# Optimization experiments

Measured on AMD Instinct MI355X. Metric: run time of the kernel, lower is better.

## Reference

```python
import jax, jax.numpy as jnp
import numpy as np

D, K, CIN, CD, COUT = 3, 16, 128, 32, 256
C = CIN + CD                  # 160 = C_in + C_delta after concat
DM = -(-COUT // C)            # depth_multiplier = ceil(C_out / C) = 2
N, I = 4, 2048                # batch, points per cloud; M = N*I = 8192


def _bn(x, g, b, eps=1e-5):
    # BatchNorm1d in training mode: biased batch statistics over dim 0
    mu = x.mean(0)
    v = x.var(0)
    return (x - mu) * jax.lax.rsqrt(v + eps) * g + b


def _knn(p, k):
    # knn_graph over ALL M points (wrapper passes no batch vector), loop=True
    d2 = jnp.sum(p * p, axis=1)
    dist = d2[:, None] + d2[None, :] - 2.0 * (p @ p.T)   # [M,M]
    _, idx = jax.lax.top_k(-dist, k)                     # [M,K], self first
    return idx


def _gconv(t, w, b, M):
    # grouped Conv1d(K, K*K, kernel=K, groups=K): t [M,K,K], w [K(cin), K(out/grp), K(tap)]
    return jnp.einsum('mcl,col->mco', t, w).reshape(M, K * K) + b


def _xconv(xf, pf, idx, w1a, b1a, g1a, be1a, w1b, b1b, g1b, be1b,
           w2, b2, g2a, be2a, wc2a, bc2a, g2b, be2b, wc2b, bc2b, g2c, be2c,
           wcd, bcd, wl, bl):
    M = pf.shape[0]
    rel = pf[idx] - pf[:, None, :]                       # [M,K,D] relative neighbor coords
    # mlp1: lift relative coords to C_delta features
    h = rel.reshape(M * K, D)
    h = _bn(jax.nn.elu(h @ w1a + b1a), g1a, be1a)
    h = _bn(jax.nn.elu(h @ w1b + b1b), g1b, be1b)
    x_star = jnp.concatenate([h.reshape(M, K, CD), xf[idx]], axis=-1)  # [M,K,C]
    x_star = x_star.transpose(0, 2, 1)                   # [M,C,K]
    # mlp2: learn KxK X-transformation from the K*D relative coords
    t = _bn(jax.nn.elu(rel.reshape(M, K * D) @ w2 + b2), g2a, be2a).reshape(M, K, K)
    t = _bn(jax.nn.elu(_gconv(t, wc2a, bc2a, M)), g2b, be2b).reshape(M, K, K)
    t = _bn(_gconv(t, wc2b, bc2b, M), g2c, be2c).reshape(M, K, K)
    xt = jnp.einsum('mck,mkj->mcj', x_star, t)           # [M,C,K] batched matmul
    # depthwise Conv1d(C, C*DM, K, groups=C) collapses K, then final Linear
    y = jnp.einsum('mcl,col->mco', xt, wcd).reshape(M, C * DM) + bcd
    return y @ wl + bl                                   # [M,COUT]


def setup_inputs() -> dict:
    key = jax.random.key(0)
    ks = jax.random.split(key, 16)
    r = lambda k, s: jax.random.normal(k, s, jnp.float32) * 0.1
    return dict(
        x=jax.random.normal(ks[0], (N, I, CIN), jnp.float32),
        pos=jax.random.normal(ks[1], (N, I, D), jnp.float32),
        w1a=r(ks[2], (D, CD)), b1a=r(ks[3], (CD,)), g1a=jnp.ones((CD,)), be1a=jnp.zeros((CD,)),
        w1b=r(ks[4], (CD, CD)), b1b=r(ks[5], (CD,)), g1b=jnp.ones((CD,)), be1b=jnp.zeros((CD,)),
        w2=r(ks[6], (D * K, K * K)), b2=r(ks[7], (K * K,)), g2a=jnp.ones((K * K,)), be2a=jnp.zeros((K * K,)),
        wc2a=r(ks[8], (K, K, K)), bc2a=r(ks[9], (K * K,)), g2b=jnp.ones((K * K,)), be2b=jnp.zeros((K * K,)),
        wc2b=r(ks[10], (K, K, K)), bc2b=r(ks[11], (K * K,)), g2c=jnp.ones((K * K,)), be2c=jnp.zeros((K * K,)),
        wcd=r(ks[12], (C, DM, K)), bcd=r(ks[13], (C * DM,)),
        wl=r(ks[14], (C * DM, COUT)), bl=r(ks[15], (COUT,)),
    )


def reference(x, pos, w1a, b1a, g1a, be1a, w1b, b1b, g1b, be1b,
              w2, b2, g2a, be2a, wc2a, bc2a, g2b, be2b, wc2b, bc2b, g2c, be2c,
              wcd, bcd, wl, bl):
    pf = pos.reshape(N * I, D)
    xf = x.reshape(N * I, CIN)
    idx = _knn(pf, K)
    out = _xconv(xf, pf, idx, w1a, b1a, g1a, be1a, w1b, b1b, g1b, be1b,
                 w2, b2, g2a, be2a, wc2a, bc2a, g2b, be2b, wc2b, bc2b, g2c, be2c,
                 wcd, bcd, wl, bl)
    return out.reshape(N, I, COUT)
```

## Files before the change

kernel.cpp:

```cpp
#include <hip/hip_runtime.h>
#include <math.h>

#define M_PTS 8192
#define MK    131072

typedef __attribute__((ext_vector_type(8))) short bf16x8;
typedef __attribute__((ext_vector_type(4))) float f32x4;
typedef __fp16 half2v __attribute__((ext_vector_type(2)));
union H2U { half2v h; unsigned u; };

__device__ __forceinline__ float elu(float v){ return v > 0.f ? v : __expf(v)-1.0f; }

__device__ __forceinline__ unsigned cvt_pk_bf16(float lo, float hi){
  unsigned r;
  asm("v_cvt_pk_bf16_f32 %0, %1, %2" : "=v"(r) : "v"(lo), "v"(hi));
  return r;
}
__device__ __forceinline__ unsigned pk_min_u16(unsigned a, unsigned b){
  unsigned r; asm("v_pk_min_u16 %0, %1, %2" : "=v"(r) : "v"(a), "v"(b)); return r;
}
__device__ __forceinline__ unsigned pk_max_u16(unsigned a, unsigned b){
  unsigned r; asm("v_pk_max_u16 %0, %1, %2" : "=v"(r) : "v"(a), "v"(b)); return r;
}

__device__ __forceinline__ unsigned distkey(float4 c, float qx, float qy, float qz, float d2q){
  #pragma clang fp contract(off)
  float dot  = __builtin_fmaf(c.z, qz, __builtin_fmaf(c.y, qy, __builtin_fmaf(c.x, qx, 0.0f)));
  float A    = d2q + c.w;
  float B    = 2.0f * dot;
  float dist = A - B;
  unsigned u = __float_as_uint(dist);
  return u ^ ((unsigned)((int)u >> 31) | 0x80000000u);
}

__global__ __launch_bounds__(256) void knn_kernel(const float* __restrict__ pos,
                                                  int* __restrict__ nidx,
                                                  float* __restrict__ st){
  __shared__ float4 cand[1024];
  __shared__ unsigned long long hits[4][2][64];
  int tid  = threadIdx.x;
  int lane = tid & 63;
  int wv   = tid >> 6;
  int q0   = blockIdx.x*8 + wv*2;
  int q1   = q0 + 1;
  if (blockIdx.x == 0){
    for (int i = tid; i < 2048; i += 256) st[i] = 0.f;
  }
  float qx0 = pos[3*q0], qy0 = pos[3*q0+1], qz0 = pos[3*q0+2];
  float qx1 = pos[3*q1], qy1 = pos[3*q1+1], qz1 = pos[3*q1+2];
  float d2q0, d2q1;
  {
    #pragma clang fp contract(off)
    d2q0 = (qx0*qx0 + qy0*qy0) + qz0*qz0;
    d2q1 = (qx1*qx1 + qy1*qy1) + qz1*qz1;
  }

  unsigned ka[8];
  #pragma unroll
  for (int s=0;s<8;s++) ka[s] = 0xFFFFFFFFu;

  for (int base = 0; base < M_PTS; base += 1024){
    for (int t = tid; t < 1024; t += 256){
      #pragma clang fp contract(off)
      int j = base + t;
      float x = pos[3*j], y = pos[3*j+1], z = pos[3*j+2];
      float d2v = (x*x + y*y) + z*z;
      cand[t] = make_float4(x,y,z,d2v);
    }
    __syncthreads();
    #pragma unroll
    for (int k=0; k<16; k++){
      float4 c = cand[lane + k*64];
      float dot0 = c.x*qx0 + c.y*qy0 + c.z*qz0;
      float dot1 = c.x*qx1 + c.y*qy1 + c.z*qz1;
      float d0 = fmaxf((d2q0 + c.w) - 2.0f*dot0, 0.f);
      float d1 = fmaxf((d2q1 + c.w) - 2.0f*dot1, 0.f);
      H2U pu; pu.h = __builtin_amdgcn_cvt_pkrtz(d0, d1);
      unsigned v = pu.u;
      #pragma unroll
      for (int s=0;s<8;s++){
        unsigned mn = pk_min_u16(v, ka[s]);
        unsigned mx = pk_max_u16(v, ka[s]);
        ka[s] = mn; v = mx;
      }
    }
    __syncthreads();
  }

  unsigned thr16[2];
  #pragma unroll
  for (int qq=0; qq<2; qq++){
    unsigned kq[8];
    #pragma unroll
    for (int s=0;s<8;s++) kq[s] = (qq==0) ? (ka[s] & 0xFFFFu) : (ka[s] >> 16);
    unsigned t16 = 0xFFFFu;
    for (int r=0; r<16; r++){
      unsigned mine = kq[0];
      unsigned best = mine;
      #pragma unroll
      for (int off=32; off>0; off>>=1){
        unsigned o = __shfl_xor(best, off, 64);
        best = min(best, o);
      }
      bool adv = (best == mine);
      #pragma unroll
      for (int s=0;s<7;s++) kq[s] = adv ? kq[s+1] : kq[s];
      kq[7] = adv ? 0xFFFFu : kq[7];
      t16 = best;
    }
    thr16[qq] = t16;
  }
  unsigned t0u = min(thr16[0] + 2u, 0x7C00u);
  unsigned t1u = min(thr16[1] + 2u, 0x7C00u);
  float thrF0, thrF1;
  asm("v_cvt_f32_f16 %0, %1" : "=v"(thrF0) : "v"(t0u));
  asm("v_cvt_f32_f16 %0, %1" : "=v"(thrF1) : "v"(t1u));

  int cnt0 = 0, cnt1 = 0;
  for (int base = 0; base < M_PTS; base += 1024){
    for (int t = tid; t < 1024; t += 256){
      #pragma clang fp contract(off)
      int j = base + t;
      float x = pos[3*j], y = pos[3*j+1], z = pos[3*j+2];
      float d2v = (x*x + y*y) + z*z;
      cand[t] = make_float4(x,y,z,d2v);
    }
    __syncthreads();
    #pragma unroll
    for (int k=0; k<16; k++){
      int j = base + lane + k*64;
      float4 c = cand[lane + k*64];
      float dot0 = c.x*qx0 + c.y*qy0 + c.z*qz0;
      float dot1 = c.x*qx1 + c.y*qy1 + c.z*qz1;
      bool h0 = ((d2q0 + c.w) - 2.0f*dot0) <= thrF0;
      bool h1 = ((d2q1 + c.w) - 2.0f*dot1) <= thrF1;
      unsigned long long m0 = __ballot(h0);
      unsigned long long m1 = __ballot(h1);
      if (m0){
        unsigned u = distkey(c, qx0, qy0, qz0, d2q0);
        if (h0){
          int slot = cnt0 + __popcll(m0 & ((1ull<<lane)-1ull));
          if (slot < 64) hits[wv][0][slot] = ((unsigned long long)u << 32) | (unsigned)j;
        }
        cnt0 += (int)__popcll(m0);
      }
      if (m1){
        unsigned u = distkey(c, qx1, qy1, qz1, d2q1);
        if (h1){
          int slot = cnt1 + __popcll(m1 & ((1ull<<lane)-1ull));
          if (slot < 64) hits[wv][1][slot] = ((unsigned long long)u << 32) | (unsigned)j;
        }
        cnt1 += (int)__popcll(m1);
      }
    }
    __syncthreads();
  }

  #pragma unroll
  for (int qq=0; qq<2; qq++){
    int cc = min(qq == 0 ? cnt0 : cnt1, 64);
    int qo = (qq == 0 ? q0 : q1)*16;
    unsigned long long mine = (lane < cc) ? hits[wv][qq][lane] : ~0ull;
    for (int r=0; r<16; r++){
      unsigned long long best = mine;
      #pragma unroll
      for (int off=32; off>0; off>>=1){
        unsigned long long o = __shfl_xor(best, off, 64);
        best = (o < best) ? o : best;
      }
      if (mine == best) mine = ~0ull;
      if (lane == 0) nidx[qo + r] = (int)(unsigned)best;
    }
  }
}

#define COMPUTE_RELF_8()                                              \
  for (int f = tid; f < 8*48; f += 256){                              \
    int p = f/48, kd = f%48, k = kd/3, d = kd%3;                      \
    int j = nidx[(m0+p)*16 + k];                                      \
    relf[p][kd] = pos[3*j+d] - pos[3*(m0+p)+d];                       \
  }                                                                   \
  __syncthreads();

#define COMPUTE_T1_8(acc)                                             \
  _Pragma("unroll")                                                   \
  for (int p=0;p<8;p++) acc[p] = b2[tid];                             \
  for (int kk=0; kk<48; kk++){                                        \
    float w = w2[kk*256 + tid];                                       \
    _Pragma("unroll")                                                 \
    for (int p=0;p<8;p++) acc[p] += relf[p][kk]*w;                    \
  }

__global__ __launch_bounds__(256) void stats_a_kernel(const float* __restrict__ pos,
    const int* __restrict__ nidx,
    const float* __restrict__ w1a, const float* __restrict__ b1a,
    const float* __restrict__ w2,  const float* __restrict__ b2,
    const float* __restrict__ wl,  unsigned short* __restrict__ wlbf,
    float* __restrict__ tact,
    float* __restrict__ s1, float* __restrict__ s3){
  int tid = threadIdx.x;
  if (blockIdx.x < 512){
    __shared__ float relS[256][3];
    __shared__ float red[8][64];
    int r = blockIdx.x*256 + tid;
    int m = r >> 4;
    int j = nidx[r];
    relS[tid][0] = pos[3*j  ]-pos[3*m  ];
    relS[tid][1] = pos[3*j+1]-pos[3*m+1];
    relS[tid][2] = pos[3*j+2]-pos[3*m+2];
    __syncthreads();
    int c = tid & 31, g = tid >> 5;
    float w0=w1a[c], w1v=w1a[32+c], w2v=w1a[64+c], b=b1a[c];
    float s=0.f, q=0.f;
    for (int rr=g*32; rr<g*32+32; rr++){
      float h = elu(b + relS[rr][0]*w0 + relS[rr][1]*w1v + relS[rr][2]*w2v);
      s += h; q += h*h;
    }
    red[g][c]=s; red[g][32+c]=q;
    __syncthreads();
    if (tid < 64){
      float a=0.f;
      #pragma unroll
      for (int gg=0;gg<8;gg++) a += red[gg][tid];
      atomicAdd(&s1[tid], a);
    }
  } else if (blockIdx.x < 1536){
    __shared__ float relf[8][48];
    int m0 = (blockIdx.x-512)*8;
    COMPUTE_RELF_8();
    float acc[8];
    COMPUTE_T1_8(acc);
    float s=0.f, q=0.f;
    #pragma unroll
    for (int p=0;p<8;p++){
      float v = elu(acc[p]);
      s += v; q += v*v;
      tact[(size_t)(m0+p)*256 + tid] = v;
    }
    atomicAdd(&s3[tid], s); atomicAdd(&s3[256+tid], q);
  } else {
    int t = (blockIdx.x - 1536)*256 + tid;
    int lane = t & 63;
    int fr   = t >> 6;
    int k0   = (fr >> 4)*32 + (lane >> 4)*8;
    int col  = (fr & 15)*16 + (lane & 15);
    const float* wp = wl + (size_t)k0*256 + col;
    uint4 v;
    v.x = cvt_pk_bf16(wp[0],    wp[256]);
    v.y = cvt_pk_bf16(wp[512],  wp[768]);
    v.z = cvt_pk_bf16(wp[1024], wp[1280]);
    v.w = cvt_pk_bf16(wp[1536], wp[1792]);
    ((uint4*)wlbf)[t] = v;
  }
}

__global__ __launch_bounds__(256) void stats_b_kernel(const float* __restrict__ pos,
    const int* __restrict__ nidx,
    const float* __restrict__ w1a, const float* __restrict__ b1a,
    const float* __restrict__ s1,  const float* __restrict__ g1a, const float* __restrict__ be1a,
    const float* __restrict__ w1b, const float* __restrict__ b1b,
    float* __restrict__ tact,
    const float* __restrict__ s3,  const float* __restrict__ g2a, const float* __restrict__ be2a,
    const float* __restrict__ wc2a,const float* __restrict__ bc2a,
    float* __restrict__ s2, float* __restrict__ s4){
  int tid = threadIdx.x;
  const float invMK = 1.f/(float)MK;
  const float invM  = 1.f/8192.f;
  if (blockIdx.x < 2048){
    __shared__ float xnS[64][33];
    __shared__ float red[8][64];
    __shared__ float muA[32], ivA[32];
    if (tid < 32){
      float mu  = s1[tid]*invMK;
      float var = s1[32+tid]*invMK - mu*mu;
      muA[tid] = mu; ivA[tid] = rsqrtf(var+1e-5f)*g1a[tid];
    }
    __syncthreads();
    {
      int rl = tid >> 2;
      int r  = blockIdx.x*64 + rl;
      int m = r >> 4;
      int j = nidx[r];
      float rx = pos[3*j]-pos[3*m], ry = pos[3*j+1]-pos[3*m+1], rz = pos[3*j+2]-pos[3*m+2];
      int c0 = (tid & 3)*8;
      #pragma unroll
      for (int u=0; u<8; u++){
        int cc = c0 + u;
        float h = elu(b1a[cc] + rx*w1a[cc] + ry*w1a[32+cc] + rz*w1a[64+cc]);
        xnS[rl][cc] = (h-muA[cc])*ivA[cc] + be1a[cc];
      }
    }
    __syncthreads();
    int o = tid & 31, g = tid >> 5;
    float wcol[32];
    #pragma unroll
    for (int cc=0;cc<32;cc++) wcol[cc] = w1b[cc*32+o];
    float bo = b1b[o], s=0.f, q=0.f;
    for (int rr=g*8; rr<g*8+8; rr++){
      float a = bo;
      #pragma unroll
      for (int cc=0;cc<32;cc++) a += xnS[rr][cc]*wcol[cc];
      float v = elu(a);
      s += v; q += v*v;
    }
    red[g][o]=s; red[g][32+o]=q;
    __syncthreads();
    if (tid < 64){
      float a=0.f;
      #pragma unroll
      for (int gg=0;gg<8;gg++) a += red[gg][tid];
      atomicAdd(&s2[tid], a);
    }
  } else {
    __shared__ float tn[8][256];
    int m0 = (blockIdx.x-2048)*8;
    float mu3  = s3[tid]*invM;
    float var3 = s3[256+tid]*invM - mu3*mu3;
    float i3   = rsqrtf(var3+1e-5f)*g2a[tid];
    float bb3  = be2a[tid];
    float tv[8];
    #pragma unroll
    for (int p=0;p<8;p++) tv[p] = tact[(size_t)(m0+p)*256 + tid];
    #pragma unroll
    for (int p=0;p<8;p++) tn[p][tid] = (tv[p]-mu3)*i3 + bb3;
    __syncthreads();
    int c = tid >> 4;
    float wreg[16];
    const float4* wv4 = (const float4*)(wc2a + tid*16);
    #pragma unroll
    for (int v=0; v<4; v++){ float4 f = wv4[v]; wreg[4*v]=f.x; wreg[4*v+1]=f.y; wreg[4*v+2]=f.z; wreg[4*v+3]=f.w; }
    float bias = bc2a[tid];
    float s=0.f, q=0.f;
    #pragma unroll
    for (int p=0;p<8;p++){
      float a2 = bias;
      #pragma unroll
      for (int l=0;l<16;l++) a2 += tn[p][c*16+l]*wreg[l];
      float v = elu(a2);
      s += v; q += v*v;
      tv[p] = v;
    }
    #pragma unroll
    for (int p=0;p<8;p++) tact[(size_t)(m0+p)*256 + tid] = tv[p];
    atomicAdd(&s4[tid], s); atomicAdd(&s4[256+tid], q);
  }
}

__global__ __launch_bounds__(256) void t3_stats_kernel(
    float* __restrict__ tact,
    const float* __restrict__ s4, const float* __restrict__ g2b, const float* __restrict__ be2b,
    const float* __restrict__ wc2b, const float* __restrict__ bc2b, float* __restrict__ s5){
  __shared__ float tn2[8][256];
  int m0 = blockIdx.x*8, tid = threadIdx.x;
  const float invM = 1.f/8192.f;
  float mu4  = s4[tid]*invM;
  float var4 = s4[256+tid]*invM - mu4*mu4;
  float i4   = rsqrtf(var4+1e-5f)*g2b[tid];
  float bb4  = be2b[tid];
  float tv[8];
  #pragma unroll
  for (int p=0;p<8;p++) tv[p] = tact[(size_t)(m0+p)*256 + tid];
  #pragma unroll
  for (int p=0;p<8;p++) tn2[p][tid] = (tv[p]-mu4)*i4 + bb4;
  __syncthreads();
  int c = tid >> 4;
  float w2reg[16];
  { const float4* wv4 = (const float4*)(wc2b + tid*16);
    #pragma unroll
    for (int v=0; v<4; v++){ float4 f = wv4[v]; w2reg[4*v]=f.x; w2reg[4*v+1]=f.y; w2reg[4*v+2]=f.z; w2reg[4*v+3]=f.w; } }
  float bias2 = bc2b[tid];
  float s=0.f, q=0.f;
  #pragma unroll
  for (int p=0;p<8;p++){
    float a3 = bias2;
    #pragma unroll
    for (int l=0;l<16;l++) a3 += tn2[p][c*16+l]*w2reg[l];
    s += a3; q += a3*a3;
    tv[p] = a3;
  }
  #pragma unroll
  for (int p=0;p<8;p++) tact[(size_t)(m0+p)*256 + tid] = tv[p];
  atomicAdd(&s5[tid], s); atomicAdd(&s5[256+tid], q);
}

#define PF8 8
__global__ __launch_bounds__(256) void final_mfma_kernel(
    const float* __restrict__ x, const float* __restrict__ pos, const int* __restrict__ nidx,
    const float* __restrict__ w1a, const float* __restrict__ b1a,
    const float* __restrict__ g1a, const float* __restrict__ be1a,
    const float* __restrict__ w1b, const float* __restrict__ b1b,
    const float* __restrict__ g1b, const float* __restrict__ be1b,
    const float* __restrict__ g2c, const float* __restrict__ be2c,
    const float* __restrict__ wcd, const float* __restrict__ bcd,
    const unsigned short* __restrict__ wlbf, const float* __restrict__ bl,
    const float* __restrict__ st,
    float* __restrict__ out){
  __shared__ float tA[PF8][256];
  __shared__ float xs[PF8*32*17];
  __shared__ unsigned short yh[16][328];
  __shared__ int   sidx[PF8*16];
  __shared__ float mu1[32], i1g[32], mu2[32], i2g[32];
  int tid = threadIdx.x;
  int m0  = blockIdx.x*PF8;
  const float invMK = 1.f/(float)MK;
  const float invM  = 1.f/8192.f;

  if (tid < PF8*16) sidx[tid] = nidx[m0*16 + tid];
  if (tid < 32){
    float mu  = st[tid]*invMK;
    float var = st[32+tid]*invMK - mu*mu;
    mu1[tid] = mu; i1g[tid] = rsqrtf(var+1e-5f)*g1a[tid];
    float mu_2  = st[64+tid]*invMK;
    float var_2 = st[96+tid]*invMK - mu_2*mu_2;
    mu2[tid] = mu_2; i2g[tid] = rsqrtf(var_2+1e-5f)*g1b[tid];
  }
  {
    unsigned short* yz = &yh[8][0];
    for (int i = tid; i < 8*328; i += 256) yz[i] = 0;
  }
  {
    float mu5 = st[1152+tid]*invM, var5 = st[1408+tid]*invM - mu5*mu5;
    float i5 = rsqrtf(var5+1e-5f)*g2c[tid], bb5 = be2c[tid];
    #pragma unroll
    for (int p=0;p<PF8;p++){
      float v = out[(size_t)(m0+p)*256 + tid];
      tA[p][tid] = (v-mu5)*i5 + bb5;
    }
  }
  __syncthreads();

  for (int half = 0; half < 2; ++half){
    int row = half*64 + (tid >> 2);
    int p = row >> 4, k = row & 15;
    int q8 = (tid & 3)*8;
    int m = m0 + p;
    int j = sidx[row];
    float rx = pos[3*j]-pos[3*m], ry = pos[3*j+1]-pos[3*m+1], rz = pos[3*j+2]-pos[3*m+2];
    float xn[32];
    #pragma unroll
    for (int cc=0; cc<32; cc++){
      float h = elu(b1a[cc] + rx*w1a[cc] + ry*w1a[32+cc] + rz*w1a[64+cc]);
      xn[cc] = (h-mu1[cc])*i1g[cc] + be1a[cc];
    }
    #pragma unroll
    for (int oo=0; oo<8; oo++){
      int o = q8 + oo;
      float a = b1b[o];
      #pragma unroll
      for (int cc=0; cc<32; cc++) a += xn[cc]*w1b[cc*32+o];
      float h2v = elu(a);
      xs[(p*32 + o)*17 + k] = (h2v-mu2[o])*i2g[o] + be1b[o];
    }
  }
  __syncthreads();

  for (int pair = tid; pair < PF8*160; pair += 256){
    int p = pair / 160, cch = pair % 160;
    float av[16];
    if (cch < 32){
      #pragma unroll
      for (int k16=0;k16<16;k16++) av[k16] = xs[(p*32+cch)*17 + k16];
    } else {
      #pragma unroll
      for (int k16=0;k16<16;k16++) av[k16] = x[(size_t)sidx[p*16+k16]*128 + (cch-32)];
    }
    float xt[16];
    #pragma unroll
    for (int j16=0;j16<16;j16++) xt[j16]=0.f;
    #pragma unroll
    for (int k16=0;k16<16;k16++){
      float a = av[k16];
      #pragma unroll
      for (int j16=0;j16<16;j16++) xt[j16] += a*tA[p][k16*16+j16];
    }
    float y0 = bcd[cch*2], y1 = bcd[cch*2+1];
    #pragma unroll
    for (int l=0;l<16;l++){
      y0 += xt[l]*wcd[cch*32 + l];
      y1 += xt[l]*wcd[cch*32 + 16 + l];
    }
    *(unsigned*)&yh[p][cch*2] = cvt_pk_bf16(y0, y1);
  }
  __syncthreads();

  {
    int lane = tid & 63;
    int wvi  = tid >> 6;
    int lrow = lane & 15;
    int lgrp = lane >> 4;
    const bf16x8* wb = (const bf16x8*)wlbf;
    f32x4 acc[4];
    #pragma unroll
    for (int nt=0; nt<4; ++nt) acc[nt] = (f32x4){0.f,0.f,0.f,0.f};
    #pragma unroll 1
    for (int kt = 0; kt < 10; ++kt){
      bf16x8 ah = *(const bf16x8*)&yh[lrow][kt*32 + lgrp*8];
      #pragma unroll
      for (int nt = 0; nt < 4; ++nt){
        bf16x8 bh = wb[(size_t)((kt*16 + wvi*4 + nt)*64) + lane];
        acc[nt] = __builtin_amdgcn_mfma_f32_16x16x32_bf16(ah, bh, acc[nt], 0, 0, 0);
      }
    }
    if (lgrp < 2){
      #pragma unroll
      for (int nt=0; nt<4; ++nt){
        int col = wvi*64 + nt*16 + lrow;
        float bv = bl[col];
        #pragma unroll
        for (int r=0;r<4;r++){
          int orow = lgrp*4 + r;
          out[(size_t)(m0+orow)*256 + col] = acc[nt][r] + bv;
        }
      }
    }
  }
}

#define PF 4
__global__ __launch_bounds__(256) void final_kernel(
    const float* __restrict__ x, const float* __restrict__ pos, const int* __restrict__ nidx,
    const float* __restrict__ w1a, const float* __restrict__ b1a,
    const float* __restrict__ g1a, const float* __restrict__ be1a,
    const float* __restrict__ w1b, const float* __restrict__ b1b,
    const float* __restrict__ g1b, const float* __restrict__ be1b,
    const float* __restrict__ g2c, const float* __restrict__ be2c,
    const float* __restrict__ wcd, const float* __restrict__ bcd,
    const float* __restrict__ wl,  const float* __restrict__ bl,
    const float* __restrict__ st,
    float* __restrict__ out){
  __shared__ float tA[PF][256];
  __shared__ float xs[PF*32*17];
  __shared__ float yy[PF][320];
  __shared__ int   sidx[PF*16];
  __shared__ float mu1[32], i1g[32], mu2[32], i2g[32];
  int tid = threadIdx.x;
  int m0  = blockIdx.x*PF;
  const float invMK = 1.f/(float)MK;
  const float invM  = 1.f/8192.f;

  if (tid < PF*16) sidx[tid] = nidx[m0*16 + tid];
  if (tid < 32){
    float mu  = st[tid]*invMK;
    float var = st[32+tid]*invMK - mu*mu;
    mu1[tid] = mu; i1g[tid] = rsqrtf(var+1e-5f)*g1a[tid];
    float mu_2  = st[64+tid]*invMK;
    float var_2 = st[96+tid]*invMK - mu_2*mu_2;
    mu2[tid] = mu_2; i2g[tid] = rsqrtf(var_2+1e-5f)*g1b[tid];
  }
  {
    float mu5 = st[1152+tid]*invM, var5 = st[1408+tid]*invM - mu5*mu5;
    float i5 = rsqrtf(var5+1e-5f)*g2c[tid], bb5 = be2c[tid];
    #pragma unroll
    for (int p=0;p<PF;p++){
      float v = out[(size_t)(m0+p)*256 + tid];
      tA[p][tid] = (v-mu5)*i5 + bb5;
    }
  }
  __syncthreads();

  {
    int row = tid >> 2;
    int p = row >> 4, k = row & 15;
    int q8 = (tid & 3)*8;
    int m = m0 + p;
    int j = sidx[p*16 + k];
    float rx = pos[3*j]-pos[3*m], ry = pos[3*j+1]-pos[3*m+1], rz = pos[3*j+2]-pos[3*m+2];
    float xn[32];
    #pragma unroll
    for (int cc=0; cc<32; cc++){
      float h = elu(b1a[cc] + rx*w1a[cc] + ry*w1a[32+cc] + rz*w1a[64+cc]);
      xn[cc] = (h-mu1[cc])*i1g[cc] + be1a[cc];
    }
    #pragma unroll
    for (int oo=0; oo<8; oo++){
      int o = q8 + oo;
      float a = b1b[o];
      #pragma unroll
      for (int cc=0; cc<32; cc++) a += xn[cc]*w1b[cc*32+o];
      float h2v = elu(a);
      xs[(p*32 + o)*17 + k] = (h2v-mu2[o])*i2g[o] + be1b[o];
    }
  }
  __syncthreads();

  for (int pair = tid; pair < PF*160; pair += 256){
    int p = pair / 160, cch = pair % 160;
    float av[16];
    if (cch < 32){
      #pragma unroll
      for (int k16=0;k16<16;k16++) av[k16] = xs[(p*32+cch)*17 + k16];
    } else {
      #pragma unroll
      for (int k16=0;k16<16;k16++) av[k16] = x[(size_t)sidx[p*16+k16]*128 + (cch-32)];
    }
    float xt[16];
    #pragma unroll
    for (int j16=0;j16<16;j16++) xt[j16]=0.f;
    #pragma unroll
    for (int k16=0;k16<16;k16++){
      float a = av[k16];
      #pragma unroll
      for (int j16=0;j16<16;j16++) xt[j16] += a*tA[p][k16*16+j16];
    }
    float y0 = bcd[cch*2], y1 = bcd[cch*2+1];
    #pragma unroll
    for (int l=0;l<16;l++){
      y0 += xt[l]*wcd[cch*32 + l];
      y1 += xt[l]*wcd[cch*32 + 16 + l];
    }
    yy[p][cch*2] = y0; yy[p][cch*2+1] = y1;
  }
  __syncthreads();

  float accO[PF];
  #pragma unroll
  for (int p=0;p<PF;p++) accO[p] = bl[tid];
  for (int q=0;q<320;q++){
    float w = wl[q*256 + tid];
    #pragma unroll
    for (int p=0;p<PF;p++) accO[p] += yy[p][q]*w;
  }
  #pragma unroll
  for (int p=0;p<PF;p++) out[(size_t)(m0+p)*256 + tid] = accO[p];
}

extern "C" void kernel_launch(void* const* d_in, const int* in_sizes, int n_in,
                              void* d_out, int out_size, void* d_ws, size_t ws_size,
                              hipStream_t stream){
  const float* x    = (const float*)d_in[0];
  const float* pos  = (const float*)d_in[1];
  const float* w1a  = (const float*)d_in[2];
  const float* b1a  = (const float*)d_in[3];
  const float* g1a  = (const float*)d_in[4];
  const float* be1a = (const float*)d_in[5];
  const float* w1b  = (const float*)d_in[6];
  const float* b1b  = (const float*)d_in[7];
  const float* g1b  = (const float*)d_in[8];
  const float* be1b = (const float*)d_in[9];
  const float* w2   = (const float*)d_in[10];
  const float* b2   = (const float*)d_in[11];
  const float* g2a  = (const float*)d_in[12];
  const float* be2a = (const float*)d_in[13];
  const float* wc2a = (const float*)d_in[14];
  const float* bc2a = (const float*)d_in[15];
  const float* g2b  = (const float*)d_in[16];
  const float* be2b = (const float*)d_in[17];
  const float* wc2b = (const float*)d_in[18];
  const float* bc2b = (const float*)d_in[19];
  const float* g2c  = (const float*)d_in[20];
  const float* be2c = (const float*)d_in[21];
  const float* wcd  = (const float*)d_in[22];
  const float* bcd  = (const float*)d_in[23];
  const float* wl   = (const float*)d_in[24];
  const float* bl   = (const float*)d_in[25];
  float* out = (float*)d_out;

  char* ws = (char*)d_ws;
  int*   nidx = (int*)(ws + 0);
  float* st   = (float*)(ws + 524288);
  float* s1 = st;
  float* s2 = st + 64;
  float* s3 = st + 128;
  float* s4 = st + 640;
  float* s5 = st + 1152;
  bool big = ws_size >= (size_t)696320;
  unsigned short* wlbf = big ? (unsigned short*)(ws + 532480) : (unsigned short*)0;

  knn_kernel<<<1024,256,0,stream>>>(pos, nidx, st);
  stats_a_kernel<<<(big ? 1576 : 1536),256,0,stream>>>(pos, nidx, w1a, b1a, w2, b2,
                                                       wl, wlbf, out, s1, s3);
  stats_b_kernel<<<3072,256,0,stream>>>(pos, nidx, w1a, b1a, s1, g1a, be1a, w1b, b1b,
                                        out, s3, g2a, be2a, wc2a, bc2a, s2, s4);
  t3_stats_kernel<<<1024,256,0,stream>>>(out, s4, g2b, be2b, wc2b, bc2b, s5);
  if (big){
    final_mfma_kernel<<<1024,256,0,stream>>>(x, pos, nidx,
                                             w1a, b1a, g1a, be1a, w1b, b1b, g1b, be1b,
                                             g2c, be2c, wcd, bcd, wlbf, bl, st, out);
  } else {
    final_kernel<<<2048,256,0,stream>>>(x, pos, nidx,
                                        w1a, b1a, g1a, be1a, w1b, b1b, g1b, be1b,
                                        g2c, be2c, wcd, bcd, wl, bl, st, out);
  }
}
```

Measured before the change: 399.6 us.

## Assign one query per wavefront in kNN, double grid, limit unrolling in final

The kNN kernel now handles one query per wavefront instead of two. The fp16 packed insertion network now keeps two independent sorted lists of candidates (lo/hi halves) for the same query, and the threshold search merges them. The grid doubles to 2048 blocks to cover all queries. This doubles the number of waves and halves per-wave register and loop work, but each candidate tile is loaded into shared memory twice as often across blocks. It also adds unroll-1 pragmas on two loops in the final kernel, likely to reduce register pressure.

```diff
diff --git a/kernel.cpp b/kernel.cpp
--- a/kernel.cpp
+++ b/kernel.cpp
@@ -37,22 +37,19 @@
                                                   int* __restrict__ nidx,
                                                   float* __restrict__ st){
   __shared__ float4 cand[1024];
-  __shared__ unsigned long long hits[4][2][64];
+  __shared__ unsigned long long hits[4][64];
   int tid  = threadIdx.x;
   int lane = tid & 63;
   int wv   = tid >> 6;
-  int q0   = blockIdx.x*8 + wv*2;
-  int q1   = q0 + 1;
+  int q    = blockIdx.x*4 + wv;
   if (blockIdx.x == 0){
     for (int i = tid; i < 2048; i += 256) st[i] = 0.f;
   }
-  float qx0 = pos[3*q0], qy0 = pos[3*q0+1], qz0 = pos[3*q0+2];
-  float qx1 = pos[3*q1], qy1 = pos[3*q1+1], qz1 = pos[3*q1+2];
-  float d2q0, d2q1;
+  float qx = pos[3*q], qy = pos[3*q+1], qz = pos[3*q+2];
+  float d2q;
   {
     #pragma clang fp contract(off)
-    d2q0 = (qx0*qx0 + qy0*qy0) + qz0*qz0;
-    d2q1 = (qx1*qx1 + qy1*qy1) + qz1*qz1;
+    d2q = (qx*qx + qy*qy) + qz*qz;
   }
 
   unsigned ka[8];
@@ -69,13 +66,14 @@
     }
     __syncthreads();
     #pragma unroll
-    for (int k=0; k<16; k++){
-      float4 c = cand[lane + k*64];
-      float dot0 = c.x*qx0 + c.y*qy0 + c.z*qz0;
-      float dot1 = c.x*qx1 + c.y*qy1 + c.z*qz1;
-      float d0 = fmaxf((d2q0 + c.w) - 2.0f*dot0, 0.f);
-      float d1 = fmaxf((d2q1 + c.w) - 2.0f*dot1, 0.f);
-      H2U pu; pu.h = __builtin_amdgcn_cvt_pkrtz(d0, d1);
+    for (int k=0; k<8; k++){
+      float4 c0 = cand[lane + k*128];
+      float4 c1 = cand[lane + 64 + k*128];
+      float dotA = c0.x*qx + c0.y*qy + c0.z*qz;
+      float dotB = c1.x*qx + c1.y*qy + c1.z*qz;
+      float dA = fmaxf((d2q + c0.w) - 2.0f*dotA, 0.f);
+      float dB = fmaxf((d2q + c1.w) - 2.0f*dotB, 0.f);
+      H2U pu; pu.h = __builtin_amdgcn_cvt_pkrtz(dA, dB);
       unsigned v = pu.u;
       #pragma unroll
       for (int s=0;s<8;s++){
@@ -87,36 +85,36 @@
     __syncthreads();
   }
 
-  unsigned thr16[2];
-  #pragma unroll
-  for (int qq=0; qq<2; qq++){
-    unsigned kq[8];
-    #pragma unroll
-    for (int s=0;s<8;s++) kq[s] = (qq==0) ? (ka[s] & 0xFFFFu) : (ka[s] >> 16);
-    unsigned t16 = 0xFFFFu;
-    for (int r=0; r<16; r++){
-      unsigned mine = kq[0];
-      unsigned best = mine;
-      #pragma unroll
-      for (int off=32; off>0; off>>=1){
-        unsigned o = __shfl_xor(best, off, 64);
-        best = min(best, o);
-      }
-      bool adv = (best == mine);
-      #pragma unroll
-      for (int s=0;s<7;s++) kq[s] = adv ? kq[s+1] : kq[s];
-      kq[7] = adv ? 0xFFFFu : kq[7];
-      t16 = best;
-    }
-    thr16[qq] = t16;
-  }
-  unsigned t0u = min(thr16[0] + 2u, 0x7C00u);
-  unsigned t1u = min(thr16[1] + 2u, 0x7C00u);
-  float thrF0, thrF1;
-  asm("v_cvt_f32_f16 %0, %1" : "=v"(thrF0) : "v"(t0u));
-  asm("v_cvt_f32_f16 %0, %1" : "=v"(thrF1) : "v"(t1u));
-
-  int cnt0 = 0, cnt1 = 0;
+  unsigned lo[8], hi[8];
+  #pragma unroll
+  for (int s=0;s<8;s++){ lo[s] = ka[s] & 0xFFFFu; hi[s] = ka[s] >> 16; }
+  unsigned t16 = 0xFFFFu;
+  for (int r=0; r<16; r++){
+    unsigned head = min(lo[0], hi[0]);
+    unsigned best = head;
+    #pragma unroll
+    for (int off=32; off>0; off>>=1){
+      unsigned o = __shfl_xor(best, off, 64);
+      best = min(best, o);
+    }
+    bool adv = (head == best);
+    bool fromLo = lo[0] <= hi[0];
+    bool aL = adv && fromLo;
+    bool aH = adv && !fromLo;
+    #pragma unroll
+    for (int s=0;s<7;s++){
+      lo[s] = aL ? lo[s+1] : lo[s];
+      hi[s] = aH ? hi[s+1] : hi[s];
+    }
+    lo[7] = aL ? 0xFFFFu : lo[7];
+    hi[7] = aH ? 0xFFFFu : hi[7];
+    t16 = best;
+  }
+  unsigned tu = min(t16 + 2u, 0x7C00u);
+  float thrF;
+  asm("v_cvt_f32_f16 %0, %1" : "=v"(thrF) : "v"(tu));
+
+  int cnt = 0;
   for (int base = 0; base < M_PTS; base += 1024){
     for (int t = tid; t < 1024; t += 256){
       #pragma clang fp contract(off)
@@ -128,49 +126,35 @@
     __syncthreads();
     #pragma unroll
     for (int k=0; k<16; k++){
-      int j = base + lane + k*64;
-      float4 c = cand[lane + k*64];
-      float dot0 = c.x*qx0 + c.y*qy0 + c.z*qz0;
-      float dot1 = c.x*qx1 + c.y*qy1 + c.z*qz1;
-      bool h0 = ((d2q0 + c.w) - 2.0f*dot0) <= thrF0;
-      bool h1 = ((d2q1 + c.w) - 2.0f*dot1) <= thrF1;
-      unsigned long long m0 = __ballot(h0);
-      unsigned long long m1 = __ballot(h1);
-      if (m0){
-        unsigned u = distkey(c, qx0, qy0, qz0, d2q0);
-        if (h0){
-          int slot = cnt0 + __popcll(m0 & ((1ull<<lane)-1ull));
-          if (slot < 64) hits[wv][0][slot] = ((unsigned long long)u << 32) | (unsigned)j;
+      int idx = lane + k*64;
+      int j = base + idx;
+      float4 c = cand[idx];
+      float dot = c.x*qx + c.y*qy + c.z*qz;
+      bool hit = ((d2q + c.w) - 2.0f*dot) <= thrF;
+      unsigned long long m = __ballot(hit);
+      if (m){
+        unsigned u = distkey(c, qx, qy, qz, d2q);
+        if (hit){
+          int slot = cnt + __popcll(m & ((1ull<<lane)-1ull));
+          if (slot < 64) hits[wv][slot] = ((unsigned long long)u << 32) | (unsigned)j;
         }
-        cnt0 += (int)__popcll(m0);
+        cnt += (int)__popcll(m);
       }
-      if (m1){
-        unsigned u = distkey(c, qx1, qy1, qz1, d2q1);
-        if (h1){
-          int slot = cnt1 + __popcll(m1 & ((1ull<<lane)-1ull));
-          if (slot < 64) hits[wv][1][slot] = ((unsigned long long)u << 32) | (unsigned)j;
-        }
-        cnt1 += (int)__popcll(m1);
-      }
-    }
-    __syncthreads();
-  }
-
-  #pragma unroll
-  for (int qq=0; qq<2; qq++){
-    int cc = min(qq == 0 ? cnt0 : cnt1, 64);
-    int qo = (qq == 0 ? q0 : q1)*16;
-    unsigned long long mine = (lane < cc) ? hits[wv][qq][lane] : ~0ull;
-    for (int r=0; r<16; r++){
-      unsigned long long best = mine;
-      #pragma unroll
-      for (int off=32; off>0; off>>=1){
-        unsigned long long o = __shfl_xor(best, off, 64);
-        best = (o < best) ? o : best;
-      }
-      if (mine == best) mine = ~0ull;
-      if (lane == 0) nidx[qo + r] = (int)(unsigned)best;
-    }
+    }
+    __syncthreads();
+  }
+
+  int cc = min(cnt, 64);
+  unsigned long long mine = (lane < cc) ? hits[wv][lane] : ~0ull;
+  for (int r=0; r<16; r++){
+    unsigned long long best = mine;
+    #pragma unroll
+    for (int off=32; off>0; off>>=1){
+      unsigned long long o = __shfl_xor(best, off, 64);
+      best = (o < best) ? o : best;
+    }
+    if (mine == best) mine = ~0ull;
+    if (lane == 0) nidx[q*16 + r] = (int)(unsigned)best;
   }
 }
 
@@ -429,6 +413,7 @@
   }
   __syncthreads();
 
+  #pragma unroll 1
   for (int half = 0; half < 2; ++half){
     int row = half*64 + (tid >> 2);
     int p = row >> 4, k = row & 15;
@@ -454,6 +439,7 @@
   }
   __syncthreads();
 
+  #pragma unroll 1
   for (int pair = tid; pair < PF8*160; pair += 256){
     int p = pair / 160, cch = pair % 160;
     float av[16];
@@ -666,7 +652,7 @@
   bool big = ws_size >= (size_t)696320;
   unsigned short* wlbf = big ? (unsigned short*)(ws + 532480) : (unsigned short*)0;
 
-  knn_kernel<<<1024,256,0,stream>>>(pos, nidx, st);
+  knn_kernel<<<2048,256,0,stream>>>(pos, nidx, st);
   stats_a_kernel<<<(big ? 1576 : 1536),256,0,stream>>>(pos, nidx, w1a, b1a, w2, b2,
                                                        wl, wlbf, out, s1, s3);
   stats_b_kernel<<<3072,256,0,stream>>>(pos, nidx, w1a, b1a, s1, g1a, be1a, w1b, b1b,
```

After: 396.4 us. About the same (-0.8%).
